# Kernel tuning notes

Hardware: AMD Instinct MI355X
Metric: run time of the kernel (lower is better)

Reference implementation:

```python
import jax, jax.numpy as jnp
import numpy as np

B, S, D = 2, 2048, 2048
H, HKV = 16, 2
DH = D // H          # 128
G = H // HKV         # 8
SCALE = float(np.sqrt(DH))


def setup_inputs() -> dict:
    key = jax.random.key(0)
    ks = jax.random.split(key, 9)
    s = 0.02
    return {
        "x":  jax.random.normal(ks[0], (B, S, D), dtype=jnp.float32),
        "Wq": jax.random.normal(ks[1], (H * DH, D), dtype=jnp.float32) * s,
        "bq": jnp.zeros((H * DH,), dtype=jnp.float32),
        "Wk": jax.random.normal(ks[2], (HKV * DH, D), dtype=jnp.float32) * s,
        "bk": jnp.zeros((HKV * DH,), dtype=jnp.float32),
        "Wv": jax.random.normal(ks[3], (HKV * DH, D), dtype=jnp.float32) * s,
        "bv": jnp.zeros((HKV * DH,), dtype=jnp.float32),
        "Wo": jax.random.normal(ks[4], (D, D), dtype=jnp.float32) * s,
        "bo": jnp.zeros((D,), dtype=jnp.float32),
    }


def reference(x, Wq, bq, Wk, bk, Wv, bv, Wo, bo):
    # projections (torch Linear: y = x @ W.T + b)
    q = (x @ Wq.T + bq).reshape(B, S, HKV, G, DH)   # grouped query heads
    k = (x @ Wk.T + bk).reshape(B, S, HKV, DH)
    v = (x @ Wv.T + bv).reshape(B, S, HKV, DH)

    # scores: [B, HKV, G, S, S]; native grouping (no KV expand/copy)
    scores = jnp.einsum('bskgd,btkd->bkgst', q, k) / SCALE

    causal = jnp.triu(jnp.ones((S, S), dtype=bool), k=1)
    scores = jnp.where(causal, -jnp.inf, scores)
    attn = jax.nn.softmax(scores, axis=-1)          # dropout = identity (eval)

    out = jnp.einsum('bkgst,btkd->bskgd', attn, v).reshape(B, S, D)
    return out @ Wo.T + bo
```

## Files before the change

kernel.cpp:

```cpp
#include <hip/hip_runtime.h>
#include <hip/hip_bf16.h>
#include <cmath>
#include <stdint.h>

#define B_ 2
#define S_ 2048
#define D_ 2048
#define H_ 16
#define HKV_ 2
#define DH_ 128
#define G_ 8
#define DKV_ 256
#define NQKV_ 2560

typedef _Float16 f16;
typedef _Float16 f16x8 __attribute__((ext_vector_type(8)));
typedef _Float16 f16x4 __attribute__((ext_vector_type(4)));
typedef float f32x4 __attribute__((ext_vector_type(4)));

__device__ __forceinline__ void gload_lds16(const void* g, void* lds) {
  __builtin_amdgcn_global_load_lds((const __attribute__((address_space(1))) void*)g,
                                   (__attribute__((address_space(3))) void*)lds,
                                   16, 0, 0);
}

__device__ __forceinline__ float fexp2(float x) {
  float r;
  asm("v_exp_f32 %0, %1" : "=v"(r) : "v"(x));
  return r;
}

__global__ void cast_kernel(const float* __restrict__ in, f16* __restrict__ out, int n4) {
  int i = blockIdx.x * blockDim.x + threadIdx.x;
  int stride = gridDim.x * blockDim.x;
  for (; i < n4; i += stride) {
    float4 v = reinterpret_cast<const float4*>(in)[i];
    f16x4 o = { (f16)v.x, (f16)v.y, (f16)v.z, (f16)v.w };
    reinterpret_cast<f16x4*>(out)[i] = o;
  }
}

template<int EPI>
__global__ __launch_bounds__(256)
void gemm_core(const f16* __restrict__ A, const f16* __restrict__ Bm,
               const float* __restrict__ bias,
               f16* __restrict__ oQ, f16* __restrict__ oK, f16* __restrict__ oV,
               float* __restrict__ oF,
               int M, int N, int K, int nbx) {
  __shared__ __align__(16) f16 sA[2][128 * 64];
  __shared__ __align__(16) f16 sB[2][128 * 64];
  const int tid  = threadIdx.x;
  const int lane = tid & 63;
  const int w    = tid >> 6;
  const int wr   = w >> 1, wc = w & 1;
  const int r16  = lane & 15, grp = lane >> 4;
  const int nwg  = gridDim.x;
  const int cpx  = nwg >> 3;
  const int lg   = (blockIdx.x & 7) * cpx + (blockIdx.x >> 3);
  const int bm   = (lg / nbx) * 128;
  const int bn   = (lg % nbx) * 128;

  f32x4 acc[4][4] = {};

  auto stage = [&](int k0, int buf) {
#pragma unroll
    for (int j = 0; j < 4; ++j) {
      int seg = j * 4 + w;
      int rr  = seg * 8 + (lane >> 3);
      int cs  = lane & 7;
      int csr = (cs ^ (rr & 7)) * 8;
      gload_lds16(A  + (size_t)(bm + rr) * K + k0 + csr, &sA[buf][seg * 512]);
      gload_lds16(Bm + (size_t)(bn + rr) * K + k0 + csr, &sB[buf][seg * 512]);
    }
  };

  stage(0, 0);
  asm volatile("s_waitcnt vmcnt(0)" ::: "memory");
  __builtin_amdgcn_s_barrier();

  const int nk = K >> 6;
  for (int t = 0; t < nk; ++t) {
    const int buf = t & 1;
    if (t + 1 < nk) stage((t + 1) << 6, buf ^ 1);

#pragma unroll
    for (int kk = 0; kk < 64; kk += 32) {
      f16x8 af[4], bf[4];
      const int cb = (kk >> 3) + grp;
      const int cx = (cb ^ (r16 & 7)) << 3;
#pragma unroll
      for (int m = 0; m < 4; ++m)
        af[m] = *reinterpret_cast<const f16x8*>(&sA[buf][(wr * 64 + m * 16 + r16) * 64 + cx]);
#pragma unroll
      for (int n = 0; n < 4; ++n)
        bf[n] = *reinterpret_cast<const f16x8*>(&sB[buf][(wc * 64 + n * 16 + r16) * 64 + cx]);
#pragma unroll
      for (int m = 0; m < 4; ++m)
#pragma unroll
        for (int n = 0; n < 4; ++n)
          acc[m][n] = __builtin_amdgcn_mfma_f32_16x16x32_f16(af[m], bf[n], acc[m][n], 0, 0, 0);
    }

    asm volatile("s_waitcnt vmcnt(0)" ::: "memory");
    __builtin_amdgcn_s_barrier();
  }

#pragma unroll
  for (int n = 0; n < 4; ++n) {
    int col = bn + wc * 64 + n * 16 + r16;
    float bv = bias ? bias[col] : 0.f;
#pragma unroll
    for (int m = 0; m < 4; ++m) {
      int row0 = bm + wr * 64 + m * 16 + grp * 4;
      if constexpr (EPI == 0) {
#pragma unroll
        for (int j = 0; j < 4; ++j)
          oF[(size_t)(row0 + j) * N + col] = acc[m][n][j] + bv;
      } else {
        if (bn < 2048) {
#pragma unroll
          for (int j = 0; j < 4; ++j)
            oQ[(size_t)(row0 + j) * 2048 + col] = (f16)(acc[m][n][j] + bv);
        } else if (bn < 2304) {
#pragma unroll
          for (int j = 0; j < 4; ++j)
            oK[(size_t)(row0 + j) * 256 + (col - 2048)] = (f16)(acc[m][n][j] + bv);
        } else {
          f16x4 st;
#pragma unroll
          for (int j = 0; j < 4; ++j) st[j] = (f16)(acc[m][n][j] + bv);
          *reinterpret_cast<f16x4*>(&oV[(size_t)(row0 >> 2) * 1024 + (col - 2304) * 4]) = st;
        }
      }
    }
  }
}

__global__ __launch_bounds__(256)
void attn_kernel(const f16* __restrict__ Q, const f16* __restrict__ K,
                 const f16* __restrict__ V4, f16* __restrict__ O) {
  __shared__ __align__(16) f16 sK[2][8192];
  __shared__ __align__(16) f16 sV[2][8192];

  const int tid  = threadIdx.x;
  const int lane = tid & 63;
  const int w    = tid >> 6;
  const int qi   = lane & 15, grp = lane >> 4;
  const int bid  = blockIdx.x;
  const int hh   = bid & 1;
  const int kvh  = (bid >> 1) & 1;
  const int b    = (bid >> 2) & 1;
  const int qt   = 127 - (bid >> 3);
  const int hq   = kvh * 8 + hh * 4 + w;
  const f16 SCL2 = (f16)(0.08838834764831845f * 1.44269504088896f);

  const f16* Kb = K  + (size_t)b * S_ * DKV_ + kvh * DH_;
  const f16* Vb = V4 + (size_t)b * S_ * DKV_ + kvh * 512;

  auto stage = [&](int t64, int buf) {
#pragma unroll
    for (int p4 = 0; p4 < 4; ++p4) {
      int ci = p4 * 256 + tid;
      int r = ci >> 4, cs = ci & 15;
      gload_lds16(Kb + (size_t)(t64 * 64 + r) * DKV_ + ((cs ^ (r & 7)) * 8),
                  (char*)&sK[buf][0] + p4 * 4096 + w * 1024);
      int g = ci >> 6, cc = ci & 63;
      gload_lds16(Vb + (size_t)(t64 * 16 + g) * 1024 + ((cc ^ g) * 8),
                  (char*)&sV[buf][0] + p4 * 4096 + w * 1024);
    }
  };

  const int nt    = (qt >> 2) + 1;
  const int q_pos = qt * 16 + qi;
  const int q_hi  = qt * 16 + 15;

  const size_t qbase = ((size_t)(b * S_ + qt * 16 + qi)) * D_ + hq * DH_;
  f16x8 qf[4];
#pragma unroll
  for (int kd = 0; kd < 4; ++kd) {
    qf[kd] = *reinterpret_cast<const f16x8*>(Q + qbase + kd * 32 + grp * 8);
#pragma unroll
    for (int e = 0; e < 8; ++e) qf[kd][e] *= SCL2;
  }

  const int q2    = qi >> 1;
  const int voff0 = ((q2 ^ grp) << 3) + (qi & 1) * 4;
  const int voff1 = ((q2 ^ (grp + 4)) << 3) + (qi & 1) * 4;

  float m = -INFINITY, lsum = 0.f;
  f32x4 accO[8] = {};

  stage(0, 0);
  asm volatile("s_waitcnt vmcnt(0)" ::: "memory");
  __builtin_amdgcn_s_barrier();

  for (int t = 0; t < nt; ++t) {
    const int buf = t & 1;
    if (t + 1 < nt) stage(t + 1, buf ^ 1);

    const bool last = (t == nt - 1);
    const f16* sVb = &sV[buf][0];
#pragma unroll
    for (int h = 0; h < 2; ++h) {
      const int kv0 = t * 64 + h * 32;
      if (kv0 > q_hi) break;
      const f16* sKh = &sK[buf][h * 32 * 128];

      f32x4 s0 = {}, s1 = {};
#pragma unroll
      for (int kd = 0; kd < 4; ++kd) {
        const int cx = ((kd * 4 + grp) ^ (qi & 7)) << 3;
        f16x8 k0 = *reinterpret_cast<const f16x8*>(sKh + qi * 128 + cx);
        f16x8 k1 = *reinterpret_cast<const f16x8*>(sKh + (16 + qi) * 128 + cx);
        s0 = __builtin_amdgcn_mfma_f32_16x16x32_f16(k0, qf[kd], s0, 0, 0, 0);
        s1 = __builtin_amdgcn_mfma_f32_16x16x32_f16(k1, qf[kd], s1, 0, 0, 0);
      }
      float p[8];
#pragma unroll
      for (int jj = 0; jj < 4; ++jj) { p[jj] = s0[jj]; p[4 + jj] = s1[jj]; }
      if (last) {
#pragma unroll
        for (int jj = 0; jj < 4; ++jj) {
          int kvp = kv0 + grp * 4 + jj;
          p[jj]     = (kvp > q_pos)      ? -INFINITY : p[jj];
          p[4 + jj] = (kvp + 16 > q_pos) ? -INFINITY : p[4 + jj];
        }
      }
      float tm = -INFINITY;
#pragma unroll
      for (int i = 0; i < 8; ++i) tm = fmaxf(tm, p[i]);
      if (!__all(tm <= m + 8.f)) {
        float r = tm;
        r = fmaxf(r, __shfl_xor(r, 16));
        r = fmaxf(r, __shfl_xor(r, 32));
        float mn = fmaxf(m, r);
        float sc = fexp2(m - mn);
        m = mn;
        lsum *= sc;
#pragma unroll
        for (int dt = 0; dt < 8; ++dt)
#pragma unroll
          for (int jj = 0; jj < 4; ++jj) accO[dt][jj] *= sc;
      }
      float ps = 0.f;
#pragma unroll
      for (int i = 0; i < 8; ++i) {
        p[i] = fexp2(p[i] - m);
        ps += p[i];
      }
      lsum += ps;

      f16x4 pf0 = { (f16)p[0], (f16)p[1], (f16)p[2], (f16)p[3] };
      f16x4 pf1 = { (f16)p[4], (f16)p[5], (f16)p[6], (f16)p[7] };
      const f16* vb0 = sVb + (h * 8 + grp) * 512 + voff0;
      const f16* vb1 = sVb + (h * 8 + grp + 4) * 512 + voff1;
#pragma unroll
      for (int dtp = 0; dtp < 8; ++dtp) {
        const int dt = dtp ^ h;
        f16x4 v0 = *reinterpret_cast<const f16x4*>(vb0 + dtp * 64);
        f16x4 v1 = *reinterpret_cast<const f16x4*>(vb1 + dtp * 64);
        accO[dt] = __builtin_amdgcn_mfma_f32_16x16x16f16(v0, pf0, accO[dt], 0, 0, 0);
        accO[dt] = __builtin_amdgcn_mfma_f32_16x16x16f16(v1, pf1, accO[dt], 0, 0, 0);
      }
    }

    asm volatile("s_waitcnt vmcnt(0)" ::: "memory");
    __builtin_amdgcn_s_barrier();
  }

  lsum += __shfl_xor(lsum, 16);
  lsum += __shfl_xor(lsum, 32);
  float inv_l = 1.f / lsum;
  const size_t obase = ((size_t)(b * S_ + qt * 16 + qi)) * D_ + hq * DH_;
#pragma unroll
  for (int dt = 0; dt < 8; ++dt) {
    f16x4 st;
#pragma unroll
    for (int jj = 0; jj < 4; ++jj) st[jj] = (f16)(accO[dt][jj] * inv_l);
    *reinterpret_cast<f16x4*>(&O[obase + dt * 16 + grp * 4]) = st;
  }
}

extern "C" void kernel_launch(void* const* d_in, const int* in_sizes, int n_in,
                              void* d_out, int out_size, void* d_ws, size_t ws_size,
                              hipStream_t stream) {
  const float* x  = (const float*)d_in[0];
  const float* Wq = (const float*)d_in[1];
  const float* bq = (const float*)d_in[2];
  const float* Wk = (const float*)d_in[3];
  const float* bk = (const float*)d_in[4];
  const float* Wv = (const float*)d_in[5];
  const float* bv = (const float*)d_in[6];
  const float* Wo = (const float*)d_in[7];
  const float* bo = (const float*)d_in[8];
  float* out = (float*)d_out;

  char* ws = (char*)d_ws;
  size_t off = 0;
  auto alloc = [&](size_t bytes) {
    char* p = ws + off;
    off += (bytes + 255) & ~(size_t)255;
    return p;
  };
  f16*   xh    = (f16*)alloc((size_t)B_ * S_ * D_ * 2);
  f16*   wqkv  = (f16*)alloc((size_t)NQKV_ * D_ * 2);
  f16*   woh   = (f16*)alloc((size_t)D_ * D_ * 2);
  f16*   qh    = (f16*)alloc((size_t)B_ * S_ * D_ * 2);
  f16*   kh    = (f16*)alloc((size_t)B_ * S_ * DKV_ * 2);
  f16*   v4h   = (f16*)alloc((size_t)B_ * S_ * DKV_ * 2);
  f16*   ah    = (f16*)alloc((size_t)B_ * S_ * D_ * 2);
  float* bqkv  = (float*)alloc((size_t)NQKV_ * 4);

  auto cast = [&](const float* in, f16* o, int n) {
    int n4 = n / 4;
    int grid = (n4 + 255) / 256;
    if (grid > 2048) grid = 2048;
    cast_kernel<<<dim3(grid), dim3(256), 0, stream>>>(in, o, n4);
  };
  cast(x,  xh, B_ * S_ * D_);
  cast(Wq, wqkv,                               D_ * D_);
  cast(Wk, wqkv + (size_t)D_ * D_,             DKV_ * D_);
  cast(Wv, wqkv + (size_t)(D_ + DKV_) * D_,    DKV_ * D_);
  cast(Wo, woh, D_ * D_);
  (void)hipMemcpyAsync(bqkv,             bq, D_ * 4,   hipMemcpyDeviceToDevice, stream);
  (void)hipMemcpyAsync(bqkv + D_,        bk, DKV_ * 4, hipMemcpyDeviceToDevice, stream);
  (void)hipMemcpyAsync(bqkv + D_ + DKV_, bv, DKV_ * 4, hipMemcpyDeviceToDevice, stream);

  const int M = B_ * S_;
  gemm_core<1><<<dim3((M / 128) * (NQKV_ / 128)), 256, 0, stream>>>(
      xh, wqkv, bqkv, qh, kh, v4h, nullptr, M, NQKV_, D_, NQKV_ / 128);

  attn_kernel<<<dim3(1024), 256, 0, stream>>>(qh, kh, v4h, ah);

  gemm_core<0><<<dim3((M / 128) * (D_ / 128)), 256, 0, stream>>>(
      ah, woh, bo, nullptr, nullptr, nullptr, out, M, D_, D_, D_ / 128);
}
```

Baseline: 213.2 us.

## Fuse cast and bias-copy launches into one prep kernel; load GEMM A directly

Five cast kernels and three device-to-device memcpys are replaced by a single prep kernel that converts x and all weights to fp16 and copies the biases into the packed bias buffer, cutting launch and copy overhead. Separately, the GEMM stops staging the A tile through LDS and has each wave read its A fragments straight from global memory. That frees half the shared memory but replaces shared LDS reuse with redundant, less coalesced global reads. The direct A loads also lose the double-buffered prefetch that hid their latency.

```diff
diff --git a/kernel.cpp b/kernel.cpp
--- a/kernel.cpp
+++ b/kernel.cpp
@@ -30,13 +30,40 @@
   return r;
 }
 
-__global__ void cast_kernel(const float* __restrict__ in, f16* __restrict__ out, int n4) {
+__global__ void prep_kernel(const float* __restrict__ x,  const float* __restrict__ Wq,
+                            const float* __restrict__ Wk, const float* __restrict__ Wv,
+                            const float* __restrict__ Wo, const float* __restrict__ bq,
+                            const float* __restrict__ bk, const float* __restrict__ bv,
+                            f16* __restrict__ xh, f16* __restrict__ wqkv,
+                            f16* __restrict__ woh, float* __restrict__ bqkv) {
+  constexpr int N0 = 2097152;
+  constexpr int N1 = N0 + 1048576;
+  constexpr int N2 = N1 + 131072;
+  constexpr int N3 = N2 + 131072;
+  constexpr int N4 = N3 + 1048576;
+  constexpr int N5 = N4 + 512;
+  constexpr int N6 = N5 + 64;
+  constexpr int N7 = N6 + 64;
   int i = blockIdx.x * blockDim.x + threadIdx.x;
-  int stride = gridDim.x * blockDim.x;
-  for (; i < n4; i += stride) {
-    float4 v = reinterpret_cast<const float4*>(in)[i];
-    f16x4 o = { (f16)v.x, (f16)v.y, (f16)v.z, (f16)v.w };
-    reinterpret_cast<f16x4*>(out)[i] = o;
+  const int stride = gridDim.x * blockDim.x;
+  for (; i < N7; i += stride) {
+    if (i < N4) {
+      const float* s; f16x4* d; int j;
+      if (i < N0)      { s = x;  d = (f16x4*)xh;             j = i; }
+      else if (i < N1) { s = Wq; d = (f16x4*)wqkv;           j = i - N0; }
+      else if (i < N2) { s = Wk; d = (f16x4*)wqkv + 1048576; j = i - N1; }
+      else if (i < N3) { s = Wv; d = (f16x4*)wqkv + 1179648; j = i - N2; }
+      else             { s = Wo; d = (f16x4*)woh;            j = i - N3; }
+      float4 v = reinterpret_cast<const float4*>(s)[j];
+      f16x4 o = { (f16)v.x, (f16)v.y, (f16)v.z, (f16)v.w };
+      d[j] = o;
+    } else {
+      const float* s; int off, j;
+      if (i < N5)      { s = bq; off = 0;   j = i - N4; }
+      else if (i < N6) { s = bk; off = 512; j = i - N5; }
+      else             { s = bv; off = 576; j = i - N6; }
+      reinterpret_cast<float4*>(bqkv)[off + j] = reinterpret_cast<const float4*>(s)[j];
+    }
   }
 }
 
@@ -47,7 +74,6 @@
                f16* __restrict__ oQ, f16* __restrict__ oK, f16* __restrict__ oV,
                float* __restrict__ oF,
                int M, int N, int K, int nbx) {
-  __shared__ __align__(16) f16 sA[2][128 * 64];
   __shared__ __align__(16) f16 sB[2][128 * 64];
   const int tid  = threadIdx.x;
   const int lane = tid & 63;
@@ -62,26 +88,28 @@
 
   f32x4 acc[4][4] = {};
 
-  auto stage = [&](int k0, int buf) {
+  auto stageB = [&](int k0, int buf) {
 #pragma unroll
     for (int j = 0; j < 4; ++j) {
       int seg = j * 4 + w;
       int rr  = seg * 8 + (lane >> 3);
       int cs  = lane & 7;
       int csr = (cs ^ (rr & 7)) * 8;
-      gload_lds16(A  + (size_t)(bm + rr) * K + k0 + csr, &sA[buf][seg * 512]);
       gload_lds16(Bm + (size_t)(bn + rr) * K + k0 + csr, &sB[buf][seg * 512]);
     }
   };
 
-  stage(0, 0);
+  const f16* Aw = A + (size_t)(bm + wr * 64 + r16) * K + grp * 8;
+
+  stageB(0, 0);
   asm volatile("s_waitcnt vmcnt(0)" ::: "memory");
   __builtin_amdgcn_s_barrier();
 
   const int nk = K >> 6;
   for (int t = 0; t < nk; ++t) {
     const int buf = t & 1;
-    if (t + 1 < nk) stage((t + 1) << 6, buf ^ 1);
+    if (t + 1 < nk) stageB((t + 1) << 6, buf ^ 1);
+    const int k0 = t << 6;
 
 #pragma unroll
     for (int kk = 0; kk < 64; kk += 32) {
@@ -90,7 +118,7 @@
       const int cx = (cb ^ (r16 & 7)) << 3;
 #pragma unroll
       for (int m = 0; m < 4; ++m)
-        af[m] = *reinterpret_cast<const f16x8*>(&sA[buf][(wr * 64 + m * 16 + r16) * 64 + cx]);
+        af[m] = *reinterpret_cast<const f16x8*>(Aw + (size_t)(m * 16) * K + k0 + kk);
 #pragma unroll
       for (int n = 0; n < 4; ++n)
         bf[n] = *reinterpret_cast<const f16x8*>(&sB[buf][(wc * 64 + n * 16 + r16) * 64 + cx]);
@@ -311,20 +339,8 @@
   f16*   ah    = (f16*)alloc((size_t)B_ * S_ * D_ * 2);
   float* bqkv  = (float*)alloc((size_t)NQKV_ * 4);
 
-  auto cast = [&](const float* in, f16* o, int n) {
-    int n4 = n / 4;
-    int grid = (n4 + 255) / 256;
-    if (grid > 2048) grid = 2048;
-    cast_kernel<<<dim3(grid), dim3(256), 0, stream>>>(in, o, n4);
-  };
-  cast(x,  xh, B_ * S_ * D_);
-  cast(Wq, wqkv,                               D_ * D_);
-  cast(Wk, wqkv + (size_t)D_ * D_,             DKV_ * D_);
-  cast(Wv, wqkv + (size_t)(D_ + DKV_) * D_,    DKV_ * D_);
-  cast(Wo, woh, D_ * D_);
-  (void)hipMemcpyAsync(bqkv,             bq, D_ * 4,   hipMemcpyDeviceToDevice, stream);
-  (void)hipMemcpyAsync(bqkv + D_,        bk, DKV_ * 4, hipMemcpyDeviceToDevice, stream);
-  (void)hipMemcpyAsync(bqkv + D_ + DKV_, bv, DKV_ * 4, hipMemcpyDeviceToDevice, stream);
+  prep_kernel<<<dim3(2048), dim3(256), 0, stream>>>(
+      x, Wq, Wk, Wv, Wo, bq, bk, bv, xh, wqkv, woh, bqkv);
 
   const int M = B_ * S_;
   gemm_core<1><<<dim3((M / 128) * (NQKV_ / 128)), 256, 0, stream>>>(
```

After: 271.8 us. +27.5%, slower.
